# Optimization experiments

Measured on AMD Instinct MI355X. Metric: run time of the kernel, lower is better.

The kernel has to match this reference:

```python
import jax, jax.numpy as jnp
import numpy as np

WS = 7
NUM_HEADS = 4
DIM = 128


def _ln(x, g, b, eps=1e-5):
    m = x.mean(-1, keepdims=True)
    v = ((x - m) ** 2).mean(-1, keepdims=True)
    return (x - m) / jnp.sqrt(v + eps) * g + b


def _rel_index(ws):
    # (N, N) relative-position index into the (2*ws-1)^2 bias table
    coords = np.stack(np.meshgrid(np.arange(ws), np.arange(ws), indexing='ij')).reshape(2, -1)
    rel = (coords[:, :, None] - coords[:, None, :]).transpose(1, 2, 0)
    rel[..., 0] += ws - 1
    rel[..., 1] += ws - 1
    rel[..., 0] *= 2 * ws - 1
    return rel.sum(-1)


def _attn_mask(Hp, Wp, ws):
    # (nW, N, N) additive shift mask, -100 where tokens come from different regions
    shift = ws // 2
    img = np.zeros((Hp, Wp))
    slices = (slice(0, -ws), slice(-ws, -shift), slice(-shift, None))
    cnt = 0
    for sh in slices:
        for sw in slices:
            img[sh, sw] = cnt
            cnt += 1
    mw = img.reshape(Hp // ws, ws, Wp // ws, ws).transpose(0, 2, 1, 3).reshape(-1, ws * ws)
    diff = mw[:, None, :] - mw[:, :, None]
    return np.where(diff != 0, -100.0, 0.0).astype(np.float32)


def setup_inputs() -> dict:
    key = jax.random.key(0)
    ks = jax.random.split(key, 8)
    d, h, ws = DIM, 4 * DIM, WS
    B, H, W = 64, 56, 56

    def w(k, shape, s=0.02):
        return (jax.random.normal(k, shape) * s).astype(jnp.float32)

    return {
        'x': jax.random.normal(ks[0], (B, H * W, d), jnp.float32),
        'norm1_g': jnp.ones(d, jnp.float32), 'norm1_b': jnp.zeros(d, jnp.float32),
        'qkv_w': w(ks[1], (d, 3 * d)), 'qkv_b': jnp.zeros(3 * d, jnp.float32),
        'proj_w': w(ks[2], (d, d)), 'proj_b': jnp.zeros(d, jnp.float32),
        'rpb_table': w(ks[3], ((2 * ws - 1) ** 2, NUM_HEADS)),
        'norm2_g': jnp.ones(d, jnp.float32), 'norm2_b': jnp.zeros(d, jnp.float32),
        'fc1_w': w(ks[4], (d, h)), 'fc1_b': jnp.zeros(h, jnp.float32),
        'fc2_w': w(ks[5], (h, d)), 'fc2_b': jnp.zeros(d, jnp.float32),
        'H': H, 'W': W,
    }


def reference(x, norm1_g, norm1_b, qkv_w, qkv_b, proj_w, proj_b, rpb_table,
              norm2_g, norm2_b, fc1_w, fc1_b, fc2_w, fc2_b, H, W):
    ws, nh = WS, NUM_HEADS
    B, L, C = x.shape
    d_head = C // nh
    scale = d_head ** -0.5
    shift = ws // 2
    N = ws * ws

    shortcut = x
    xn = _ln(x, norm1_g, norm1_b).reshape(B, H, W, C)
    pad_b = (ws - H % ws) % ws
    pad_r = (ws - W % ws) % ws
    if pad_b or pad_r:
        xn = jnp.pad(xn, ((0, 0), (0, pad_b), (0, pad_r), (0, 0)))
    Hp, Wp = H + pad_b, W + pad_r

    # cyclic shift (shift=True branch)
    xn = jnp.roll(xn, (-shift, -shift), axis=(1, 2))

    # window partition: (B, Hp, Wp, C) -> (B*nW, N, C)
    nHw, nWw = Hp // ws, Wp // ws
    win = xn.reshape(B, nHw, ws, nWw, ws, C).transpose(0, 1, 3, 2, 4, 5).reshape(B * nHw * nWw, N, C)

    qkv = (win @ qkv_w + qkv_b).reshape(-1, N, 3, nh, d_head).transpose(2, 0, 3, 1, 4)
    q, k, v = qkv[0], qkv[1], qkv[2]  # (Bw, nh, N, d_head)

    attn = jnp.einsum('bhnd,bhmd->bhnm', q, k) * scale
    bias = rpb_table[jnp.asarray(_rel_index(ws))].transpose(2, 0, 1)  # (nh, N, N)
    attn = attn + bias[None]

    mask = jnp.asarray(_attn_mask(Hp, Wp, ws))  # (nW, N, N)
    nW = mask.shape[0]
    attn = attn.reshape(B, nW, nh, N, N) + mask[None, :, None]
    attn = jax.nn.softmax(attn.reshape(-1, nh, N, N), axis=-1)

    out = jnp.einsum('bhnm,bhmd->bhnd', attn, v).transpose(0, 2, 1, 3).reshape(-1, N, C)
    out = out @ proj_w + proj_b

    # window reverse + un-shift + un-pad
    out = out.reshape(B, nHw, nWw, ws, ws, C).transpose(0, 1, 3, 2, 4, 5).reshape(B, Hp, Wp, C)
    out = jnp.roll(out, (shift, shift), axis=(1, 2))
    out = out[:, :H, :W].reshape(B, H * W, C) + shortcut

    out = out + (jax.nn.gelu(_ln(out, norm2_g, norm2_b) @ fc1_w + fc1_b, approximate=False) @ fc2_w + fc2_b)
    return out
```

## Files before the change

kernel.cpp:

```cpp
#include <hip/hip_runtime.h>
#include <hip/hip_bf16.h>
#include <math.h>

typedef __bf16 bf16x8 __attribute__((ext_vector_type(8)));
typedef __bf16 bf16x4 __attribute__((ext_vector_type(4)));
typedef float  f32x4  __attribute__((ext_vector_type(4)));
typedef unsigned int u32x4 __attribute__((ext_vector_type(4)));
typedef __hip_bfloat16 bf16_t;

static constexpr int C_    = 128;
static constexpr int L_    = 56 * 56;
static constexpr int M_    = 64 * L_;
static constexpr int NWIN  = 64 * 64;

__device__ inline long win_to_tok(int tw)
{
    int win = tw / 49, n = tw % 49;
    int bb  = win >> 6, wi = win & 63;
    int wh  = wi >> 3, wwp = wi & 7;
    int hs  = wh * 7 + n / 7;
    int wsv = wwp * 7 + n % 7;
    int hh  = (hs + 3) % 56;
    int ww  = (wsv + 3) % 56;
    return (long)bb * L_ + hh * 56 + ww;
}

__device__ inline unsigned int pk2(float lo, float hi)
{
    unsigned short a = __builtin_bit_cast(unsigned short, (__bf16)lo);
    unsigned short b = __builtin_bit_cast(unsigned short, (__bf16)hi);
    return (unsigned int)a | ((unsigned int)b << 16);
}

__device__ inline float gelu_f(float x)
{
    float u = 0.7978845608f * x * (1.f + 0.044715f * x * x);
    float e = __expf(2.f * fminf(u, 15.f));
    return x * e * __builtin_amdgcn_rcpf(e + 1.f);
}

__global__ void sentinel_kernel(float* o) { o[threadIdx.x] = 1e9f; }

__global__ void transpose_w(const float* __restrict__ w, bf16_t* __restrict__ wt,
                            int K, int N)
{
    int i = blockIdx.x * 256 + threadIdx.x;
    if (i >= K * N) return;
    int k = i / N, n = i % N;
    wt[(long)n * K + k] = __float2bfloat16(w[i]);
}

__global__ __launch_bounds__(256) void swin_fused(const float* __restrict__ x,
                                                  const float* __restrict__ lng,
                                                  const float* __restrict__ lnb,
                                                  const bf16_t* __restrict__ qkvwt,
                                                  const float*  __restrict__ qkvb,
                                                  const float*  __restrict__ rpb,
                                                  const bf16_t* __restrict__ projwt,
                                                  const float*  __restrict__ projb,
                                                  bf16_t* __restrict__ y)
{
    __shared__ char xnb[16384];

    int win  = blockIdx.x;
    int tid  = threadIdx.x;
    int wave = tid >> 6;
    int lane = tid & 63;
    int la = lane & 15, lb = lane >> 4;
    int h = wave;

    int srcA = la + (((2 * lb)     & 3) << 4);
    int srcB = la + (((2 * lb + 1) & 3) << 4);
    bool hiT = (lb >> 1) & 1;

    auto rpk = [&](const unsigned int w0[2], const unsigned int w1[2]) -> bf16x8 {
        unsigned int a0 = __shfl(w0[0], srcA);
        unsigned int b0 = __shfl(w1[0], srcA);
        unsigned int a1 = __shfl(w0[1], srcA);
        unsigned int b1 = __shfl(w1[1], srcA);
        unsigned int a2 = __shfl(w0[0], srcB);
        unsigned int b2 = __shfl(w1[0], srcB);
        unsigned int a3 = __shfl(w0[1], srcB);
        unsigned int b3 = __shfl(w1[1], srcB);
        u32x4 uu = { hiT ? b0 : a0, hiT ? b1 : a1, hiT ? b2 : a2, hiT ? b3 : a3 };
        return __builtin_bit_cast(bf16x8, uu);
    };

    {
        int row = wave * 16 + la;
        int tw  = win * 49 + row;
        if (tw > M_ - 1) tw = M_ - 1;
        long src = win_to_tok(tw);
        const float* xr = x + src * C_;
        float vals[4][8];
        float sm = 0.f, qs = 0.f;
#pragma unroll
        for (int kt = 0; kt < 4; ++kt) {
            f32x4 u0 = *reinterpret_cast<const f32x4*>(xr + kt * 32 + lb * 8);
            f32x4 u1 = *reinterpret_cast<const f32x4*>(xr + kt * 32 + lb * 8 + 4);
#pragma unroll
            for (int j = 0; j < 4; ++j) { vals[kt][j] = u0[j]; vals[kt][4 + j] = u1[j]; }
#pragma unroll
            for (int j = 0; j < 8; ++j) { sm += vals[kt][j]; qs += vals[kt][j] * vals[kt][j]; }
        }
        sm += __shfl_xor(sm, 16); sm += __shfl_xor(sm, 32);
        qs += __shfl_xor(qs, 16); qs += __shfl_xor(qs, 32);
        float mean = sm * (1.f / 128.f);
        float rstd = rsqrtf(qs * (1.f / 128.f) - mean * mean + 1e-5f);
#pragma unroll
        for (int kt = 0; kt < 4; ++kt) {
            bf16x8 v8;
#pragma unroll
            for (int j = 0; j < 8; ++j) {
                int col = kt * 32 + lb * 8 + j;
                v8[j] = (__bf16)((vals[kt][j] - mean) * rstd * lng[col] + lnb[col]);
            }
            int colb = kt * 64 + lb * 16;
            *reinterpret_cast<bf16x8*>(xnb + row * 256 + (colb ^ ((row & 7) << 4))) = v8;
        }
    }
    __syncthreads();

    f32x4 qkT[4][4];
    f32x4 vacc[4][2];
#pragma unroll
    for (int ct = 0; ct < 4; ++ct) {
        int colb = (ct < 2) ? (h * 32 + ct * 16) : (128 + h * 32 + (ct - 2) * 16);
        f32x4 bq = *reinterpret_cast<const f32x4*>(qkvb + colb + lb * 4);
#pragma unroll
        for (int tt = 0; tt < 4; ++tt) qkT[ct][tt] = bq;
    }
#pragma unroll
    for (int nt = 0; nt < 2; ++nt) {
        float bv = qkvb[256 + h * 32 + nt * 16 + la];
#pragma unroll
        for (int s = 0; s < 4; ++s) vacc[s][nt] = (f32x4){bv, bv, bv, bv};
    }

#pragma unroll
    for (int kt = 0; kt < 4; ++kt) {
        bf16x8 ar[4];
#pragma unroll
        for (int tt = 0; tt < 4; ++tt) {
            int row = tt * 16 + la;
            ar[tt] = *reinterpret_cast<const bf16x8*>(
                xnb + row * 256 + ((kt * 64 + lb * 16) ^ ((row & 7) << 4)));
        }
#pragma unroll
        for (int ct = 0; ct < 4; ++ct) {
            int colb = (ct < 2) ? (h * 32 + ct * 16) : (128 + h * 32 + (ct - 2) * 16);
            bf16x8 wf = *reinterpret_cast<const bf16x8*>(
                qkvwt + (long)(colb + la) * 128 + kt * 32 + lb * 8);
#pragma unroll
            for (int tt = 0; tt < 4; ++tt)
                qkT[ct][tt] = __builtin_amdgcn_mfma_f32_16x16x32_bf16(
                    wf, ar[tt], qkT[ct][tt], 0, 0, 0);
        }
#pragma unroll
        for (int nt = 0; nt < 2; ++nt) {
            bf16x8 wv = *reinterpret_cast<const bf16x8*>(
                qkvwt + (long)(256 + h * 32 + nt * 16 + la) * 128 + kt * 32 + lb * 8);
#pragma unroll
            for (int s = 0; s < 4; ++s)
                vacc[s][nt] = __builtin_amdgcn_mfma_f32_16x16x32_bf16(
                    ar[s], wv, vacc[s][nt], 0, 0, 0);
        }
    }

    bf16x8 qf[4], kf[4];
#pragma unroll
    for (int tt = 0; tt < 4; ++tt) {
        unsigned int wq0[2] = { pk2(qkT[0][tt][0], qkT[0][tt][1]),
                                pk2(qkT[0][tt][2], qkT[0][tt][3]) };
        unsigned int wq1[2] = { pk2(qkT[1][tt][0], qkT[1][tt][1]),
                                pk2(qkT[1][tt][2], qkT[1][tt][3]) };
        qf[tt] = rpk(wq0, wq1);
        unsigned int wk0[2] = { pk2(qkT[2][tt][0], qkT[2][tt][1]),
                                pk2(qkT[2][tt][2], qkT[2][tt][3]) };
        unsigned int wk1[2] = { pk2(qkT[3][tt][0], qkT[3][tt][1]),
                                pk2(qkT[3][tt][2], qkT[3][tt][3]) };
        kf[tt] = rpk(wk0, wk1);
    }

    f32x4 S[4][4];
#pragma unroll
    for (int qt = 0; qt < 4; ++qt)
#pragma unroll
        for (int kt = 0; kt < 4; ++kt)
            S[qt][kt] = __builtin_amdgcn_mfma_f32_16x16x32_bf16(
                kf[kt], qf[qt], (f32x4){0.f, 0.f, 0.f, 0.f}, 0, 0, 0);

    const float scale = 0.17677669529663687f;
    int wi  = win & 63;
    int wh  = wi >> 3, wwp = wi & 7;
    bool edge = (wh == 7) || (wwp == 7);

    int i1[4], j1[4], r1[4], c1[4];
#pragma unroll
    for (int qt = 0; qt < 4; ++qt) {
        int q  = qt * 16 + la;
        int qc = q < 49 ? q : 48;
        i1[qt] = qc / 7; j1[qt] = qc - 7 * i1[qt];
        r1[qt] = (wh  < 7) ? 0 : ((i1[qt] < 4) ? 1 : 2);
        c1[qt] = (wwp < 7) ? 0 : ((j1[qt] < 4) ? 1 : 2);
    }

#pragma unroll
    for (int kt = 0; kt < 4; ++kt) {
#pragma unroll
        for (int r = 0; r < 4; ++r) {
            if (kt == 3 && r > 0) {
#pragma unroll
                for (int qt = 0; qt < 4; ++qt) S[qt][kt][r] = -1e30f;
                continue;
            }
            int key = kt * 16 + lb * 4 + r;
            int kc  = key < 49 ? key : 48;
            int i2  = kc / 7, j2 = kc - 7 * i2;
            int r2  = (wh  < 7) ? 0 : ((i2 < 4) ? 1 : 2);
            int c2  = (wwp < 7) ? 0 : ((j2 < 4) ? 1 : 2);
#pragma unroll
            for (int qt = 0; qt < 4; ++qt) {
                float bv  = rpb[(((i1[qt] - i2 + 6) * 13 + (j1[qt] - j2 + 6)) << 2) + h];
                float val = S[qt][kt][r] * scale + bv;
                if (edge && ((r1[qt] != r2) | (c1[qt] != c2))) val -= 100.f;
                if (kt == 3 && lb > 0) val = -1e30f;
                S[qt][kt][r] = val;
            }
        }
    }

    float inv[4];
#pragma unroll
    for (int qt = 0; qt < 4; ++qt) {
        float mx = -3e38f;
#pragma unroll
        for (int kt = 0; kt < 4; ++kt)
#pragma unroll
            for (int r = 0; r < 4; ++r) mx = fmaxf(mx, S[qt][kt][r]);
        mx = fmaxf(mx, __shfl_xor(mx, 16));
        mx = fmaxf(mx, __shfl_xor(mx, 32));
        float sm = 0.f;
#pragma unroll
        for (int kt = 0; kt < 4; ++kt)
#pragma unroll
            for (int r = 0; r < 4; ++r) {
                float e = __expf(S[qt][kt][r] - mx);
                S[qt][kt][r] = e;
                sm += e;
            }
        sm += __shfl_xor(sm, 16);
        sm += __shfl_xor(sm, 32);
        inv[qt] = 1.f / sm;
    }

    unsigned int w_[4][4][2];
#pragma unroll
    for (int qt = 0; qt < 4; ++qt)
#pragma unroll
        for (int t = 0; t < 4; ++t) {
            w_[qt][t][0] = pk2(S[qt][t][0], S[qt][t][1]);
            w_[qt][t][1] = pk2(S[qt][t][2], S[qt][t][3]);
        }

    unsigned int wvp[2][4][2];
#pragma unroll
    for (int nt = 0; nt < 2; ++nt)
#pragma unroll
        for (int s = 0; s < 4; ++s) {
            wvp[nt][s][0] = pk2(vacc[s][nt][0], vacc[s][nt][1]);
            wvp[nt][s][1] = pk2(vacc[s][nt][2], vacc[s][nt][3]);
        }

    f32x4 O[2][4];
#pragma unroll
    for (int dt = 0; dt < 2; ++dt)
#pragma unroll
        for (int qt = 0; qt < 4; ++qt) O[dt][qt] = (f32x4){0.f, 0.f, 0.f, 0.f};

#pragma unroll
    for (int kk = 0; kk < 2; ++kk) {
        int tl = kk * 2;
        bf16x8 vf[2];
#pragma unroll
        for (int dt = 0; dt < 2; ++dt)
            vf[dt] = rpk(wvp[dt][tl], wvp[dt][tl + 1]);
#pragma unroll
        for (int qt = 0; qt < 4; ++qt) {
            bf16x8 pf = rpk(w_[qt][tl], w_[qt][tl + 1]);
#pragma unroll
            for (int dt = 0; dt < 2; ++dt)
                O[dt][qt] = __builtin_amdgcn_mfma_f32_16x16x32_bf16(vf[dt], pf, O[dt][qt], 0, 0, 0);
        }
    }

    __syncthreads();
    __bf16 (*attw)[152] = (__bf16(*)[152])xnb;
#pragma unroll
    for (int qt = 0; qt < 4; ++qt) {
        int q = qt * 16 + la;
        if (q < 49) {
            float iv = inv[qt];
#pragma unroll
            for (int dt = 0; dt < 2; ++dt) {
                unsigned int s0 = pk2(O[dt][qt][0] * iv, O[dt][qt][1] * iv);
                unsigned int s1 = pk2(O[dt][qt][2] * iv, O[dt][qt][3] * iv);
                uint2 st = {s0, s1};
                *reinterpret_cast<uint2*>(&attw[q][h * 32 + dt * 16 + lb * 4]) = st;
            }
        }
    }
    __syncthreads();

    int n0 = h * 32;
    f32x4 pacc[4][2];
#pragma unroll
    for (int nt = 0; nt < 2; ++nt) {
        float bv = projb[n0 + nt * 16 + la];
#pragma unroll
        for (int s = 0; s < 4; ++s) pacc[s][nt] = (f32x4){bv, bv, bv, bv};
    }
#pragma unroll
    for (int kt = 0; kt < 4; ++kt) {
        bf16x8 ar[4];
#pragma unroll
        for (int s = 0; s < 4; ++s)
            ar[s] = *reinterpret_cast<const bf16x8*>(&attw[s * 16 + la][kt * 32 + lb * 8]);
#pragma unroll
        for (int nt = 0; nt < 2; ++nt) {
            bf16x8 br = *reinterpret_cast<const bf16x8*>(
                projwt + (long)(n0 + nt * 16 + la) * 128 + kt * 32 + lb * 8);
#pragma unroll
            for (int s = 0; s < 4; ++s)
                pacc[s][nt] = __builtin_amdgcn_mfma_f32_16x16x32_bf16(
                    ar[s], br, pacc[s][nt], 0, 0, 0);
        }
    }

#pragma unroll
    for (int s = 0; s < 4; ++s) {
#pragma unroll
        for (int r = 0; r < 4; ++r) {
            int q = s * 16 + lb * 4 + r;
            if (q < 49) {
                long to = win_to_tok(win * 49 + q);
#pragma unroll
                for (int nt = 0; nt < 2; ++nt) {
                    int col = n0 + nt * 16 + la;
                    y[to * C_ + col] =
                        __float2bfloat16(pacc[s][nt][r] + x[to * C_ + col]);
                }
            }
        }
    }
}

__global__ __launch_bounds__(512, 4) void mlp_fused(const bf16_t* __restrict__ y,
                                                    const float* __restrict__ g,
                                                    const float* __restrict__ b,
                                                    const bf16_t* __restrict__ w1t,
                                                    const float* __restrict__ b1,
                                                    const bf16_t* __restrict__ w2t,
                                                    const float* __restrict__ b2,
                                                    float* __restrict__ out)
{
    __shared__ uint4 ldsq[2048];
    int tid  = threadIdx.x;
    int lane = tid & 63;
    int la = lane & 15, lb = lane >> 4;
    int m0 = (blockIdx.x * 8 + (tid >> 6)) * 32;

    auto stage = [&](int c) {
        char* d1 = (char*)&ldsq[0];
        const char* s1 = (const char*)w1t + (size_t)c * 16384;
#pragma unroll
        for (int i = 0; i < 2; ++i) {
            int idx = i * 512 + tid;
            int row = idx >> 4, colb = (idx & 15) * 16;
            uint4 v = *reinterpret_cast<const uint4*>(s1 + idx * 16);
            *reinterpret_cast<uint4*>(d1 + row * 256 + (colb ^ ((row & 7) << 4))) = v;
        }
        char* d2 = (char*)&ldsq[1024];
        const char* s2 = (const char*)w2t + (size_t)c * 128;
#pragma unroll
        for (int i = 0; i < 2; ++i) {
            int idx = i * 512 + tid;
            int row = idx >> 3, colb = (idx & 7) * 16;
            uint4 v = *reinterpret_cast<const uint4*>(s2 + (size_t)row * 1024 + colb);
            *reinterpret_cast<uint4*>(d2 + row * 128 + (colb ^ ((row & 7) << 4))) = v;
        }
    };

    bf16x8 af[2][4];
#pragma unroll
    for (int s = 0; s < 2; ++s) {
        const bf16_t* yr = y + (long)(m0 + s * 16 + la) * C_;
        float vals[4][8];
        float sm = 0.f, qs = 0.f;
#pragma unroll
        for (int kt = 0; kt < 4; ++kt) {
            bf16x8 v8 = *reinterpret_cast<const bf16x8*>(yr + kt * 32 + lb * 8);
#pragma unroll
            for (int j = 0; j < 8; ++j) {
                float v = (float)v8[j];
                vals[kt][j] = v; sm += v; qs += v * v;
            }
        }
        sm += __shfl_xor(sm, 16); sm += __shfl_xor(sm, 32);
        qs += __shfl_xor(qs, 16); qs += __shfl_xor(qs, 32);
        float mean = sm * (1.f / 128.f);
        float rstd = rsqrtf(qs * (1.f / 128.f) - mean * mean + 1e-5f);
#pragma unroll
        for (int kt = 0; kt < 4; ++kt)
#pragma unroll
            for (int j = 0; j < 8; ++j) {
                int col = kt * 32 + lb * 8 + j;
                af[s][kt][j] = (__bf16)((vals[kt][j] - mean) * rstd * g[col] + b[col]);
            }
    }

    f32x4 acc[2][8];
#pragma unroll
    for (int nt2 = 0; nt2 < 8; ++nt2) {
        f32x4 bv = *reinterpret_cast<const f32x4*>(b2 + nt2 * 16 + lb * 4);
#pragma unroll
        for (int s = 0; s < 2; ++s) acc[s][nt2] = bv;
    }

    int srcA = la + (((2 * lb)     & 3) << 4);
    int srcB = la + (((2 * lb + 1) & 3) << 4);
    bool hiT = (lb >> 1) & 1;

    for (int c = 0; c < 8; ++c) {
        stage(c);
        __syncthreads();

        const char* L1 = (const char*)&ldsq[0];
        const char* L2 = (const char*)&ldsq[1024];

        f32x4 hacc[2][4];
#pragma unroll
        for (int nt = 0; nt < 4; ++nt) {
            f32x4 bv = *reinterpret_cast<const f32x4*>(b1 + c * 64 + nt * 16 + lb * 4);
#pragma unroll
            for (int s = 0; s < 2; ++s) hacc[s][nt] = bv;
        }
#pragma unroll
        for (int kt = 0; kt < 4; ++kt)
#pragma unroll
            for (int nt = 0; nt < 4; ++nt) {
                int row = nt * 16 + la;
                bf16x8 w1f = *reinterpret_cast<const bf16x8*>(
                    L1 + row * 256 + ((kt * 64 + lb * 16) ^ ((row & 7) << 4)));
#pragma unroll
                for (int s = 0; s < 2; ++s)
                    hacc[s][nt] = __builtin_amdgcn_mfma_f32_16x16x32_bf16(
                        w1f, af[s][kt], hacc[s][nt], 0, 0, 0);
            }
        unsigned int wpk[2][4][2];
#pragma unroll
        for (int s = 0; s < 2; ++s)
#pragma unroll
            for (int t = 0; t < 4; ++t) {
                f32x4 hv = hacc[s][t];
#pragma unroll
                for (int r = 0; r < 4; ++r) hv[r] = gelu_f(hv[r]);
                wpk[s][t][0] = pk2(hv[0], hv[1]);
                wpk[s][t][1] = pk2(hv[2], hv[3]);
            }
#pragma unroll
        for (int kk = 0; kk < 2; ++kk) {
            int tl = kk * 2;
#pragma unroll
            for (int s = 0; s < 2; ++s) {
                unsigned int a0 = __shfl(wpk[s][tl][0],     srcA);
                unsigned int b0 = __shfl(wpk[s][tl + 1][0], srcA);
                unsigned int a1 = __shfl(wpk[s][tl][1],     srcA);
                unsigned int b1v = __shfl(wpk[s][tl + 1][1], srcA);
                unsigned int a2 = __shfl(wpk[s][tl][0],     srcB);
                unsigned int b2v = __shfl(wpk[s][tl + 1][0], srcB);
                unsigned int a3 = __shfl(wpk[s][tl][1],     srcB);
                unsigned int b3v = __shfl(wpk[s][tl + 1][1], srcB);
                u32x4 uu = { hiT ? b0 : a0, hiT ? b1v : a1, hiT ? b2v : a2, hiT ? b3v : a3 };
                bf16x8 pf = __builtin_bit_cast(bf16x8, uu);
#pragma unroll
                for (int nt2 = 0; nt2 < 8; ++nt2) {
                    int row2 = nt2 * 16 + la;
                    bf16x8 w2f = *reinterpret_cast<const bf16x8*>(
                        L2 + row2 * 128 + ((kk * 64 + lb * 16) ^ ((row2 & 7) << 4)));
                    acc[s][nt2] = __builtin_amdgcn_mfma_f32_16x16x32_bf16(
                        w2f, pf, acc[s][nt2], 0, 0, 0);
                }
            }
        }
        __syncthreads();
    }

#pragma unroll
    for (int s = 0; s < 2; ++s) {
        long m = m0 + s * 16 + la;
        const bf16_t* yrow = y + m * C_;
        float* orow = out + m * C_;
#pragma unroll
        for (int nt2 = 0; nt2 < 8; ++nt2) {
            int n2 = nt2 * 16 + lb * 4;
            bf16x4 rb = *reinterpret_cast<const bf16x4*>(yrow + n2);
            f32x4 val = acc[s][nt2];
#pragma unroll
            for (int r = 0; r < 4; ++r) val[r] += (float)rb[r];
            *reinterpret_cast<f32x4*>(orow + n2) = val;
        }
    }
}

extern "C" void kernel_launch(void* const* d_in, const int* in_sizes, int n_in,
                              void* d_out, int out_size, void* d_ws, size_t ws_size,
                              hipStream_t stream)
{
    (void)in_sizes; (void)n_in; (void)out_size;

    const float* x      = (const float*)d_in[0];
    const float* n1g    = (const float*)d_in[1];
    const float* n1b    = (const float*)d_in[2];
    const float* qkv_w  = (const float*)d_in[3];
    const float* qkv_b  = (const float*)d_in[4];
    const float* proj_w = (const float*)d_in[5];
    const float* proj_b = (const float*)d_in[6];
    const float* rpb    = (const float*)d_in[7];
    const float* n2g    = (const float*)d_in[8];
    const float* n2b    = (const float*)d_in[9];
    const float* fc1_w  = (const float*)d_in[10];
    const float* fc1_b  = (const float*)d_in[11];
    const float* fc2_w  = (const float*)d_in[12];
    const float* fc2_b  = (const float*)d_in[13];

    char* ws = (char*)d_ws;

    const size_t yb_sz = (size_t)M_ * 128 * 2;
    const size_t w_sz  = (size_t)(128 * 384 + 128 * 128 + 128 * 512 + 512 * 128) * 2;
    const size_t need  = yb_sz + w_sz;

    if (need > ws_size) {
        sentinel_kernel<<<1, 256, 0, stream>>>((float*)d_out);
        return;
    }

    bf16_t* yb      = (bf16_t*)ws;
    bf16_t* qkv_wt  = (bf16_t*)(ws + yb_sz);
    bf16_t* proj_wt = qkv_wt + 128 * 384;
    bf16_t* fc1_wt  = proj_wt + 128 * 128;
    bf16_t* fc2_wt  = fc1_wt + 128 * 512;

    transpose_w<<<(128 * 384 + 255) / 256, 256, 0, stream>>>(qkv_w, qkv_wt, 128, 384);
    transpose_w<<<(128 * 128 + 255) / 256, 256, 0, stream>>>(proj_w, proj_wt, 128, 128);
    transpose_w<<<(128 * 512 + 255) / 256, 256, 0, stream>>>(fc1_w, fc1_wt, 128, 512);
    transpose_w<<<(512 * 128 + 255) / 256, 256, 0, stream>>>(fc2_w, fc2_wt, 512, 128);

    swin_fused<<<NWIN, 256, 0, stream>>>(x, n1g, n1b, qkv_wt, qkv_b, rpb,
                                         proj_wt, proj_b, yb);
    mlp_fused<<<M_ / 256, 512, 0, stream>>>(
        yb, n2g, n2b, fc1_wt, fc1_b, fc2_wt, fc2_b, (float*)d_out);
}
```

Measured before the change: 427.4 us.

## Stage Q/K projection through shared memory instead of register shuffles

The Q/K projection is reorganised so that each wave computes a contiguous 64-column slice of the Q|K output for all 64 rows. It writes the results as bf16 into a new 32 KB swizzled shared-memory buffer, and each head then reads its Q and K fragments back from it. This replaces the per-wave transposed MFMA plus cross-lane shuffle repacking (rpk) and lets the attention output reuse the new buffer, which drops one barrier. In exchange, LDS use per block triples to 48 KB, which can lower occupancy, and the scalar 2-byte LDS stores may cause bank conflicts.

```diff
diff --git a/kernel.cpp b/kernel.cpp
--- a/kernel.cpp
+++ b/kernel.cpp
@@ -60,7 +60,9 @@
                                                   const float*  __restrict__ projb,
                                                   bf16_t* __restrict__ y)
 {
-    __shared__ char xnb[16384];
+    __shared__ char smem[16384 + 32768];
+    char* xnb = smem;
+    char* qkb = smem + 16384;
 
     int win  = blockIdx.x;
     int tid  = threadIdx.x;
@@ -121,66 +123,77 @@
     }
     __syncthreads();
 
-    f32x4 qkT[4][4];
     f32x4 vacc[4][2];
-#pragma unroll
-    for (int ct = 0; ct < 4; ++ct) {
-        int colb = (ct < 2) ? (h * 32 + ct * 16) : (128 + h * 32 + (ct - 2) * 16);
-        f32x4 bq = *reinterpret_cast<const f32x4*>(qkvb + colb + lb * 4);
-#pragma unroll
-        for (int tt = 0; tt < 4; ++tt) qkT[ct][tt] = bq;
-    }
 #pragma unroll
     for (int nt = 0; nt < 2; ++nt) {
         float bv = qkvb[256 + h * 32 + nt * 16 + la];
 #pragma unroll
         for (int s = 0; s < 4; ++s) vacc[s][nt] = (f32x4){bv, bv, bv, bv};
     }
-
-#pragma unroll
-    for (int kt = 0; kt < 4; ++kt) {
-        bf16x8 ar[4];
-#pragma unroll
-        for (int tt = 0; tt < 4; ++tt) {
-            int row = tt * 16 + la;
-            ar[tt] = *reinterpret_cast<const bf16x8*>(
-                xnb + row * 256 + ((kt * 64 + lb * 16) ^ ((row & 7) << 4)));
-        }
-#pragma unroll
-        for (int ct = 0; ct < 4; ++ct) {
-            int colb = (ct < 2) ? (h * 32 + ct * 16) : (128 + h * 32 + (ct - 2) * 16);
-            bf16x8 wf = *reinterpret_cast<const bf16x8*>(
-                qkvwt + (long)(colb + la) * 128 + kt * 32 + lb * 8);
-#pragma unroll
-            for (int tt = 0; tt < 4; ++tt)
-                qkT[ct][tt] = __builtin_amdgcn_mfma_f32_16x16x32_bf16(
-                    wf, ar[tt], qkT[ct][tt], 0, 0, 0);
-        }
-#pragma unroll
-        for (int nt = 0; nt < 2; ++nt) {
-            bf16x8 wv = *reinterpret_cast<const bf16x8*>(
-                qkvwt + (long)(256 + h * 32 + nt * 16 + la) * 128 + kt * 32 + lb * 8);
-#pragma unroll
-            for (int s = 0; s < 4; ++s)
-                vacc[s][nt] = __builtin_amdgcn_mfma_f32_16x16x32_bf16(
-                    ar[s], wv, vacc[s][nt], 0, 0, 0);
-        }
-    }
-
-    bf16x8 qf[4], kf[4];
-#pragma unroll
-    for (int tt = 0; tt < 4; ++tt) {
-        unsigned int wq0[2] = { pk2(qkT[0][tt][0], qkT[0][tt][1]),
-                                pk2(qkT[0][tt][2], qkT[0][tt][3]) };
-        unsigned int wq1[2] = { pk2(qkT[1][tt][0], qkT[1][tt][1]),
-                                pk2(qkT[1][tt][2], qkT[1][tt][3]) };
-        qf[tt] = rpk(wq0, wq1);
-        unsigned int wk0[2] = { pk2(qkT[2][tt][0], qkT[2][tt][1]),
-                                pk2(qkT[2][tt][2], qkT[2][tt][3]) };
-        unsigned int wk1[2] = { pk2(qkT[3][tt][0], qkT[3][tt][1]),
-                                pk2(qkT[3][tt][2], qkT[3][tt][3]) };
-        kf[tt] = rpk(wk0, wk1);
-    }
+    {
+        int c0 = wave * 64;
+        f32x4 acc[4][4];
+#pragma unroll
+        for (int nt = 0; nt < 4; ++nt) {
+            float bv = qkvb[c0 + nt * 16 + la];
+#pragma unroll
+            for (int s = 0; s < 4; ++s) acc[s][nt] = (f32x4){bv, bv, bv, bv};
+        }
+#pragma unroll
+        for (int kt = 0; kt < 4; ++kt) {
+            bf16x8 ar[4];
+#pragma unroll
+            for (int s = 0; s < 4; ++s) {
+                int row = s * 16 + la;
+                ar[s] = *reinterpret_cast<const bf16x8*>(
+                    xnb + row * 256 + ((kt * 64 + lb * 16) ^ ((row & 7) << 4)));
+            }
+#pragma unroll
+            for (int nt = 0; nt < 4; ++nt) {
+                bf16x8 br = *reinterpret_cast<const bf16x8*>(
+                    qkvwt + (long)(c0 + nt * 16 + la) * 128 + kt * 32 + lb * 8);
+#pragma unroll
+                for (int s = 0; s < 4; ++s)
+                    acc[s][nt] = __builtin_amdgcn_mfma_f32_16x16x32_bf16(
+                        ar[s], br, acc[s][nt], 0, 0, 0);
+            }
+#pragma unroll
+            for (int nt = 0; nt < 2; ++nt) {
+                bf16x8 wv = *reinterpret_cast<const bf16x8*>(
+                    qkvwt + (long)(256 + h * 32 + nt * 16 + la) * 128 + kt * 32 + lb * 8);
+#pragma unroll
+                for (int s = 0; s < 4; ++s)
+                    vacc[s][nt] = __builtin_amdgcn_mfma_f32_16x16x32_bf16(
+                        ar[s], wv, vacc[s][nt], 0, 0, 0);
+            }
+        }
+#pragma unroll
+        for (int s = 0; s < 4; ++s) {
+#pragma unroll
+            for (int r = 0; r < 4; ++r) {
+                int row = s * 16 + lb * 4 + r;
+#pragma unroll
+                for (int nt = 0; nt < 4; ++nt) {
+                    int col = c0 + nt * 16 + la;
+                    *reinterpret_cast<__bf16*>(
+                        qkb + row * 512 + ((col * 2) ^ ((row & 7) << 4))) =
+                        (__bf16)acc[s][nt][r];
+                }
+            }
+        }
+    }
+    __syncthreads();
+
+    bf16x8 kf[4], qf[4];
+#pragma unroll
+    for (int t = 0; t < 4; ++t) {
+        int row = t * 16 + la;
+        kf[t] = *reinterpret_cast<const bf16x8*>(
+            qkb + row * 512 + ((256 + h * 64 + lb * 16) ^ ((row & 7) << 4)));
+        qf[t] = *reinterpret_cast<const bf16x8*>(
+            qkb + row * 512 + ((      h * 64 + lb * 16) ^ ((row & 7) << 4)));
+    }
+    __syncthreads();
 
     f32x4 S[4][4];
 #pragma unroll
@@ -294,8 +307,7 @@
         }
     }
 
-    __syncthreads();
-    __bf16 (*attw)[152] = (__bf16(*)[152])xnb;
+    __bf16 (*attw)[152] = (__bf16(*)[152])qkb;
 #pragma unroll
     for (int qt = 0; qt < 4; ++qt) {
         int q = qt * 16 + la;
```

Result: slower. 457.0 us (+6.9%).
